# Optimization experiments

Hardware: AMD Instinct MI355X
Metric: run time of the kernel (lower is better)

Reference implementation:

```python
import jax, jax.numpy as jnp
import numpy as np

NHID = 256
NHEADS = 8
HEAD_F = NHID // NHEADS  # GAT per-head out_features
ALPHA = 0.1              # GAT LeakyReLU slope
NEG = -9e15


def _leaky(x, slope):
    return jnp.where(x >= 0, x, slope * x)


def _cnorm(x, axis):
    # matches Norm.compute_norm: (x - mean) / (std_unbiased + 1e-6)
    m = jnp.mean(x, axis=axis, keepdims=True)
    s = jnp.std(x, axis=axis, keepdims=True, ddof=1)
    return (x - m) / (s + 1e-6)


def _norm(x):
    # Norm('bn') forward: per-sample normalize over features (dim=1 of x[i]) then nodes (dim=0)
    return _cnorm(_cnorm(x, axis=2), axis=1)


def setup_inputs() -> dict:
    key = jax.random.key(0)
    ks = jax.random.split(key, 12)
    B, N, E, H, D = 4, 1024, NHID, NHEADS, HEAD_F

    def xavier(k, shape, gain=1.414):
        fan_in, fan_out = shape[-2], shape[-1]
        a = gain * np.sqrt(6.0 / (fan_in + fan_out))
        return jax.random.uniform(k, shape, jnp.float32, -a, a)

    return {
        "x": jax.random.normal(ks[0], (B, N, E), jnp.float32),
        "src": jax.random.normal(ks[1], (N, B, E), jnp.float32),
        "adj": jax.random.randint(ks[2], (B, N, N), 0, 2, jnp.int32),
        "Wg": xavier(ks[3], (H, E, D)),                 # per-head GAT W
        "a1": xavier(ks[4], (H, D, 1))[..., 0],         # a[:D]
        "a2": xavier(ks[5], (H, D, 1))[..., 0],         # a[D:]
        "lin_w": xavier(ks[6], (E, E), gain=1.0),
        "lin_b": jnp.zeros((E,), jnp.float32),
        "in_proj_w": xavier(ks[7], (3 * E, E), gain=1.0),
        "in_proj_b": jnp.zeros((3 * E,), jnp.float32),
        "out_proj_w": xavier(ks[8], (E, E), gain=1.0),
        "out_proj_b": jnp.zeros((E,), jnp.float32),
    }


def reference(x, src, adj, Wg, a1, a2, lin_w, lin_b, in_proj_w, in_proj_b, out_proj_w, out_proj_b):
    B, N, E = x.shape
    H, D = NHEADS, HEAD_F

    # --- multi-head dense GAT (all heads vectorized) ---
    Wh = jnp.einsum("bnf,hfd->hbnd", x, Wg)                      # [H,B,N,D]
    s1 = jnp.einsum("hbnd,hd->hbn", Wh, a1)                      # a1 . Wh_i
    s2 = jnp.einsum("hbnd,hd->hbn", Wh, a2)                      # a2 . Wh_j
    e = _leaky(s1[..., :, None] + s2[..., None, :], ALPHA)       # [H,B,N,N]
    e = jnp.where(adj[None] > 0, e, NEG)
    attn = jax.nn.softmax(e, axis=-1)                            # [H,B,N,N]
    hp = _leaky(jnp.einsum("hbnm,hbmd->hbnd", attn, Wh), 0.01)   # F.leaky_relu default

    x = x + jnp.transpose(hp, (1, 2, 0, 3)).reshape(B, N, H * D)
    e_out = jnp.mean(attn, axis=0)                               # [B,N,N]

    # --- norm1 -> linear -> norm2 ---
    x = _norm(x) @ lin_w.T + lin_b
    x = _norm(x)

    # --- nn.MultiheadAttention(query=x, key=x, value=src) ---
    srcb = jnp.transpose(src, (1, 0, 2))                         # [B,N,E]
    Wq, Wk, Wv = in_proj_w[:E], in_proj_w[E:2 * E], in_proj_w[2 * E:]
    bq, bk, bv = in_proj_b[:E], in_proj_b[E:2 * E], in_proj_b[2 * E:]
    Dh = E // H
    q = (x @ Wq.T + bq).reshape(B, N, H, Dh)
    k = (x @ Wk.T + bk).reshape(B, N, H, Dh)
    v = (srcb @ Wv.T + bv).reshape(B, N, H, Dh)
    scores = jnp.einsum("bqhd,bkhd->bhqk", q, k) / jnp.sqrt(jnp.float32(Dh))
    p = jax.nn.softmax(scores, axis=-1)
    o = jnp.einsum("bhqk,bkhd->bqhd", p, v).reshape(B, N, E)
    x = o @ out_proj_w.T + out_proj_b                            # [B,N,E]

    return (x, e_out)
```

## Files before the change

kernel.cpp:

```cpp
#include <hip/hip_runtime.h>
#include <hip/hip_bf16.h>

#define BIAS_OFF 196608
#define S1_OFF   198400
#define S2_OFF   231168
#define CS_OFF   263936
#define ST1_OFF  296704
#define ST2_OFF  298752
#define A_OFF    300800
#define MX_OFF   825088
#define RS_OFF   857856
#define PK_OFF   890624
#define B_OFF    1349376
#define C_OFF    2397952
#define FLAG_F   3446528

#define NEGC (-9.0e15f)

typedef __attribute__((ext_vector_type(8))) short bf16x8s;
typedef __attribute__((ext_vector_type(4))) float f32x4;

static __device__ __forceinline__ float bf2f(unsigned short u) {
  union { unsigned int i; float f; } v; v.i = ((unsigned int)u) << 16; return v.f;
}
static __device__ __forceinline__ unsigned short f2bf(float f) {
  union { float f; unsigned int u; } v; v.f = f;
  unsigned int r = (v.u + 0x7FFFu + ((v.u >> 16) & 1u)) >> 16;
  return (unsigned short)r;
}
static __device__ __forceinline__ float ldin(const void* p, long i, int bf) {
  return bf ? bf2f(((const unsigned short*)p)[i]) : ((const float*)p)[i];
}
static __device__ __forceinline__ unsigned short rdbf(const void* p, long i, int bf) {
  if (bf) return ((const unsigned short*)p)[i];
  return f2bf(((const float*)p)[i]);
}
static __device__ __forceinline__ void stout(void* p, long i, float v, int bf) {
  if (bf) ((unsigned short*)p)[i] = f2bf(v);
  else    ((float*)p)[i] = v;
}

__global__ __launch_bounds__(64) void detect_kernel(const unsigned short* x, int* flag) {
  int lane = threadIdx.x;
  unsigned short u = x[2 * lane];
  int e = (u >> 7) & 0xFF;
  bool good = (e >= 100 && e <= 140);
  unsigned long long m = __ballot(good);
  if (lane == 0) *flag = (__popcll(m) >= 48) ? 1 : 0;
}

__global__ __launch_bounds__(256) void packadj_kernel(const int* adj,
                                                      unsigned long long* pk) {
  int t = threadIdx.x, w = t >> 6, lane = t & 63;
  long row = blockIdx.x;
  #pragma unroll
  for (int j = 0; j < 4; ++j) {
    int m = t + 256*j;
    bool bit = adj[row*1024 + m] > 0;
    unsigned long long mask = __ballot(bit);
    if (lane == 0) pk[row*16 + w + 4*j] = mask;
  }
}

__global__ __launch_bounds__(256) void prep_kernel(
    const void* wg, const void* lin_w, const void* inp_w, const void* out_w,
    const void* lin_b, const void* inp_b, const void* out_b,
    const void* a1, const void* a2, float* ws, const int* flagp) {
  const int bf = *flagp;
  unsigned short* wbf = (unsigned short*)ws;
  int t = threadIdx.x;
  int f = blockIdx.x;
  int m = blockIdx.y;
  int dst = m*65536 + ((f >> 2)*256 + t)*4 + (f & 3);
  if (m == 0) {
    int h = t >> 5, d = t & 31;
    wbf[dst] = rdbf(wg, h*8192 + f*32 + d, bf);
  } else if (m == 1) wbf[dst] = rdbf(lin_w, t*256 + f, bf);
  else if (m == 2)   wbf[dst] = rdbf(inp_w, t*256 + f, bf);
  else if (m == 3)   wbf[dst] = rdbf(inp_w, (256 + t)*256 + f, bf);
  else if (m == 4)   wbf[dst] = rdbf(inp_w, (512 + t)*256 + f, bf);
  else if (m == 5)   wbf[dst] = rdbf(out_w, t*256 + f, bf);
  else if (f == 0) {
    ws[BIAS_OFF + t]        = ldin(lin_b, t, bf);
    ws[BIAS_OFF + 256 + t]  = ldin(inp_b, t, bf);
    ws[BIAS_OFF + 512 + t]  = ldin(inp_b, 256 + t, bf);
    ws[BIAS_OFF + 768 + t]  = ldin(inp_b, 512 + t, bf);
    ws[BIAS_OFF + 1024 + t] = ldin(out_b, t, bf);
    ws[BIAS_OFF + 1280 + t] = ldin(a1, t, bf);
    ws[BIAS_OFF + 1536 + t] = ldin(a2, t, bf);
  }
}

__global__ __launch_bounds__(256) void whs_kernel(const void* x, float* ws,
                                                  const int* flagp) {
  const int bf = *flagp;
  int t = threadIdx.x;
  int r0 = blockIdx.x * 8;
  __shared__ __align__(16) float U[8][256];
  #pragma unroll
  for (int r = 0; r < 8; ++r)
    U[r][t] = ldin(x, (long)(r0 + r)*256 + t, bf);
  __syncthreads();
  const ushort4* w4 = (const ushort4*)ws;
  float acc[8] = {0,0,0,0,0,0,0,0};
  for (int e4 = 0; e4 < 64; ++e4) {
    ushort4 u = w4[e4*256 + t];
    float w0 = bf2f(u.x), w1 = bf2f(u.y), w2 = bf2f(u.z), w3 = bf2f(u.w);
    #pragma unroll
    for (int r = 0; r < 8; ++r) {
      float4 uu = *(const float4*)&U[r][e4*4];
      acc[r] += uu.x*w0 + uu.y*w1 + uu.z*w2 + uu.w*w3;
    }
  }
  int h = t >> 5, d = t & 31;
  float a1v = ws[BIAS_OFF + 1280 + t];
  float a2v = ws[BIAS_OFF + 1536 + t];
  unsigned short wvals[8];
  #pragma unroll
  for (int r = 0; r < 8; ++r) {
    int row = r0 + r;
    wvals[r] = f2bf(acc[r]);
    float p1 = acc[r]*a1v, p2 = acc[r]*a2v;
    #pragma unroll
    for (int off = 16; off > 0; off >>= 1) {
      p1 += __shfl_xor(p1, off, 32);
      p2 += __shfl_xor(p2, off, 32);
    }
    if (d == 0) {
      ws[S1_OFF + h*4096 + row] = p1;
      ws[S2_OFF + h*4096 + row] = p2;
    }
  }
  {
    unsigned short* wht = (unsigned short*)(ws + A_OFF);
    int bb = r0 >> 10, nn = r0 & 1023;
    *(bf16x8s*)(wht + ((long)((h*4 + bb)*32 + d))*1024 + nn) = *(bf16x8s*)wvals;
  }
}

#define PB_S 1032
__global__ __launch_bounds__(512) void attn1a_kernel(const void* x, float* ws,
                                                     const int* flagp) {
  const int bf = *flagp;
  int t = threadIdx.x;
  int gid = blockIdx.x;
  int h = gid & 7;
  int b = (gid >> 3) & 3;
  int n0 = (gid >> 5) * 16;
  __shared__ __align__(16) float s2s[1024];
  __shared__ __align__(16) unsigned short Pb[16][PB_S];
  __shared__ __align__(16) float opart[8][16][17];
  int w = t >> 6, lane = t & 63;
  int m = lane & 15, quad = lane >> 4;
  const unsigned long long* pk = (const unsigned long long*)(ws + PK_OFF);
  const float* s2p = ws + S2_OFF + h*4096 + b*1024;
  #pragma unroll
  for (int j = 0; j < 2; ++j) s2s[t + 512*j] = s2p[t + 512*j];
  __syncthreads();
  #pragma unroll
  for (int rr = 0; rr < 2; ++rr) {
    int r = 2*w + rr;
    int rowi = __builtin_amdgcn_readfirstlane(b*1024 + n0 + r);
    const unsigned long long* prow = pk + (long)rowi * 16;
    float s1v = ws[S1_OFF + h*4096 + rowi];
    float p[16];
    float mx = -3.4e38f;
    #pragma unroll
    for (int j = 0; j < 16; ++j) {
      int mm = lane + 64*j;
      float ev = s1v + s2s[mm];
      ev = (ev >= 0.0f) ? ev : 0.1f*ev;
      ev = ((prow[j] >> lane) & 1ull) ? ev : NEGC;
      p[j] = ev;
      mx = fmaxf(mx, ev);
    }
    #pragma unroll
    for (int off = 32; off > 0; off >>= 1) mx = fmaxf(mx, __shfl_xor(mx, off));
    float s = 0.0f;
    #pragma unroll
    for (int j = 0; j < 16; ++j) { p[j] = __expf(p[j] - mx); s += p[j]; }
    #pragma unroll
    for (int off = 32; off > 0; off >>= 1) s += __shfl_xor(s, off);
    float rs = 1.0f / s;
    #pragma unroll
    for (int j = 0; j < 16; ++j)
      Pb[r][lane + 64*j] = f2bf(p[j] * rs);
    if (lane == 0) {
      ws[MX_OFF + h*4096 + rowi] = mx;
      ws[RS_OFF + h*4096 + rowi] = rs;
    }
  }
  __syncthreads();
  {
    const unsigned short* wht = (const unsigned short*)(ws + A_OFF);
    int ntile = w & 1;
    int ktbase = (w >> 1) * 8;
    int vd = ntile*16 + m;
    const unsigned short* wrow = wht + ((long)((h*4 + b)*32 + vd))*1024;
    f32x4 acc0 = {0.0f, 0.0f, 0.0f, 0.0f};
    f32x4 acc1 = {0.0f, 0.0f, 0.0f, 0.0f};
    #pragma unroll
    for (int kt2 = 0; kt2 < 4; ++kt2) {
      int kt = ktbase + 2*kt2;
      bf16x8s ap0 = *(const bf16x8s*)&Pb[m][kt*32 + quad*8];
      bf16x8s bw0 = *(const bf16x8s*)(wrow + kt*32 + quad*8);
      acc0 = __builtin_amdgcn_mfma_f32_16x16x32_bf16(ap0, bw0, acc0, 0, 0, 0);
      bf16x8s ap1 = *(const bf16x8s*)&Pb[m][(kt+1)*32 + quad*8];
      bf16x8s bw1 = *(const bf16x8s*)(wrow + (kt+1)*32 + quad*8);
      acc1 = __builtin_amdgcn_mfma_f32_16x16x32_bf16(ap1, bw1, acc1, 0, 0, 0);
    }
    f32x4 acc = acc0 + acc1;
    #pragma unroll
    for (int i = 0; i < 4; ++i)
      opart[w][quad*4 + i][m] = acc[i];
  }
  __syncthreads();
  {
    int r = t >> 5, dd = t & 31;
    int nt = dd >> 4, c = dd & 15;
    float sum = opart[nt][r][c] + opart[nt + 2][r][c]
              + opart[nt + 4][r][c] + opart[nt + 6][r][c];
    float hv = (sum >= 0.0f) ? sum : 0.01f*sum;
    long idx = (long)(b*1024 + n0 + r)*256 + h*32 + dd;
    ws[C_OFF + idx] = ldin(x, idx, bf) + hv;
  }
}

__global__ __launch_bounds__(256) void eout_kernel(float* ws, void* dout,
                                                   const int* flagp) {
  const int bf = *flagp;
  int t = threadIdx.x;
  int gid = blockIdx.x;
  int b = gid & 3;
  int n = gid >> 2;
  int row = b*1024 + n;
  int w = t >> 6, lane = t & 63;
  __shared__ float part[8];
  const unsigned long long* pk = (const unsigned long long*)(ws + PK_OFF);
  const unsigned long long* prow = pk + (long)row * 16;
  float v = ws[C_OFF + (long)row*256 + t];
  float s = v;
  #pragma unroll
  for (int off = 32; off > 0; off >>= 1) s += __shfl_xor(s, off);
  if (lane == 0) part[w] = s;
  __syncthreads();
  float mean = (part[0] + part[1] + part[2] + part[3]) * (1.0f/256.0f);
  float d = v - mean;
  float ss = d*d;
  #pragma unroll
  for (int off = 32; off > 0; off >>= 1) ss += __shfl_xor(ss, off);
  if (lane == 0) part[4 + w] = ss;
  __syncthreads();
  float inv = 1.0f / (sqrtf((part[4]+part[5]+part[6]+part[7]) * (1.0f/255.0f)) + 1e-6f);
  ws[B_OFF + (long)row*256 + t] = d * inv;
  float s1v[8], mxv[8], rsv[8];
  #pragma unroll
  for (int h = 0; h < 8; ++h) {
    s1v[h] = ws[S1_OFF + h*4096 + row];
    mxv[h] = ws[MX_OFF + h*4096 + row];
    rsv[h] = ws[RS_OFF + h*4096 + row];
  }
  const float* s2b = ws + S2_OFF + b*1024;
  #pragma unroll
  for (int j = 0; j < 4; ++j) {
    int m = t + 256*j;
    bool a = (prow[w + 4*j] >> lane) & 1ull;
    float acc = 0.0f;
    #pragma unroll
    for (int h = 0; h < 8; ++h) {
      float ev = s1v[h] + s2b[h*4096 + m];
      ev = (ev >= 0.0f) ? ev : 0.1f*ev;
      ev = a ? ev : NEGC;
      acc += rsv[h] * __expf(ev - mxv[h]);
    }
    stout(dout, 1048576L + (long)row*1024 + m, 0.125f*acc, bf);
  }
}

__global__ __launch_bounds__(256) void colstatsA_kernel(const float* in, float* cs) {
  int t = threadIdx.x;
  int j = blockIdx.x & 15;
  int b = blockIdx.x >> 4;
  float s = 0, ss = 0;
  for (int n = j*64; n < j*64 + 64; ++n) {
    float v = in[(b*1024 + n)*256 + t];
    s += v; ss += v*v;
  }
  cs[(b*16 + j)*256 + t] = s;
  cs[16384 + (b*16 + j)*256 + t] = ss;
}

__global__ __launch_bounds__(256) void colstatsB_kernel(const float* cs, float* st) {
  int t = threadIdx.x;
  int b = blockIdx.x;
  float s = 0, ss = 0;
  for (int j = 0; j < 16; ++j) {
    s  += cs[(b*16 + j)*256 + t];
    ss += cs[16384 + (b*16 + j)*256 + t];
  }
  float mean = s * (1.0f/1024.0f);
  float var = fmaxf((ss - s*mean) * (1.0f/1023.0f), 0.0f);
  st[b*256 + t] = mean;
  st[1024 + b*256 + t] = 1.0f / (sqrtf(var) + 1e-6f);
}

template<int IN_MODE, int RN, int OUTM, int ROWS>
__global__ __launch_bounds__(256) void gemm_kernel(const void* inp,
    const unsigned short* wmat, const float* bias, const float* st, void* outp,
    const int* flagp) {
  const int bf = *flagp;
  int t = threadIdx.x;
  int r0 = blockIdx.x * ROWS;
  __shared__ __align__(16) float U[ROWS][256];
  #pragma unroll
  for (int r = 0; r < ROWS; ++r) {
    int row = r0 + r;
    float v;
    if (IN_MODE == 0) {
      v = ((const float*)inp)[row*256 + t];
    } else if (IN_MODE == 1) {
      int b = row >> 10;
      v = (((const float*)inp)[row*256 + t] - st[b*256 + t]) * st[1024 + b*256 + t];
    } else if (IN_MODE == 2) {
      int b = row >> 10, n = row & 1023;
      v = ldin(inp, (long)(n*4 + b)*256 + t, bf);
    } else {
      int b = row >> 10, n = row & 1023;
      v = ((const float*)inp)[((b*8 + (t >> 5))*1024 + n)*32 + (t & 31)];
    }
    U[r][t] = v;
  }
  __syncthreads();
  float bv = bias[t];
  float acc[ROWS];
  #pragma unroll
  for (int r = 0; r < ROWS; ++r) acc[r] = bv;
  const ushort4* w4 = (const ushort4*)wmat;
  for (int e4 = 0; e4 < 64; ++e4) {
    ushort4 u = w4[e4*256 + t];
    float w0 = bf2f(u.x), w1 = bf2f(u.y), w2 = bf2f(u.z), w3 = bf2f(u.w);
    #pragma unroll
    for (int r = 0; r < ROWS; ++r) {
      float4 uu = *(const float4*)&U[r][e4*4];
      acc[r] += uu.x*w0 + uu.y*w1 + uu.z*w2 + uu.w*w3;
    }
  }
  if (RN == 0) {
    #pragma unroll
    for (int r = 0; r < ROWS; ++r) {
      int row = r0 + r;
      if (OUTM == 0) ((float*)outp)[row*256 + t] = acc[r];
      else if (OUTM == 1) stout(outp, (long)row*256 + t, acc[r], bf);
      else if (OUTM == 2) {
        int b = row >> 10, n = row & 1023;
        ((float*)outp)[((b*8 + (t >> 5))*1024 + n)*32 + (t & 31)] = acc[r];
      } else if (OUTM == 3) {
        int b = row >> 10, n = row & 1023;
        ((unsigned short*)outp)[((b*8 + (t >> 5))*1024 + n)*32 + (t & 31)] = f2bf(acc[r]);
      } else {
        int b = row >> 10, n = row & 1023;
        ((unsigned short*)outp)[((b*8 + (t >> 5))*32 + (t & 31))*1024 + n] = f2bf(acc[r]);
      }
    }
  } else {
    __syncthreads();
    #pragma unroll
    for (int r = 0; r < ROWS; ++r) U[r][t] = acc[r];
    __syncthreads();
    int w = t >> 6, lane = t & 63;
    for (int rr = w; rr < ROWS; rr += 4) {
      float vals[4]; float s = 0.0f;
      #pragma unroll
      for (int j = 0; j < 4; ++j) { vals[j] = U[rr][lane + 64*j]; s += vals[j]; }
      #pragma unroll
      for (int off = 32; off > 0; off >>= 1) s += __shfl_xor(s, off);
      float mean = s * (1.0f/256.0f);
      float ss = 0.0f;
      #pragma unroll
      for (int j = 0; j < 4; ++j) { float d = vals[j] - mean; ss += d*d; }
      #pragma unroll
      for (int off = 32; off > 0; off >>= 1) ss += __shfl_xor(ss, off);
      float inv = 1.0f / (sqrtf(ss * (1.0f/255.0f)) + 1e-6f);
      #pragma unroll
      for (int j = 0; j < 4; ++j)
        ((float*)outp)[(r0 + rr)*256 + lane + 64*j] = (vals[j] - mean) * inv;
    }
  }
}

#define SPS 1036
__global__ __launch_bounds__(512) void attn2_kernel(float* ws) {
  int t = threadIdx.x;
  int gid = blockIdx.x;
  int h = gid & 7;
  int b = (gid >> 3) & 3;
  int n0 = (gid >> 5) << 4;
  __shared__ __align__(16) float Sp[16*SPS];
  __shared__ __align__(16) float opart[8][16][17];
  float* qq = ws + A_OFF;
  const unsigned short* kk = (const unsigned short*)(ws + B_OFF);
  const unsigned short* vt = (const unsigned short*)(ws + C_OFF);
  int base_bh = (b*8 + h)*1024;
  int w = t >> 6, lane = t & 63;
  int m = lane & 15, quad = lane >> 4;
  const float scl = 0.17677669529663687f;
  {
    const float* qp = qq + (base_bh + n0 + m)*32 + quad*8;
    bf16x8s aq;
    #pragma unroll
    for (int j = 0; j < 8; ++j) ((unsigned short*)&aq)[j] = f2bf(qp[j]);
    f32x4 zero = {0.0f, 0.0f, 0.0f, 0.0f};
    #pragma unroll
    for (int kt = 0; kt < 8; ++kt) {
      int kbase = w*128 + kt*16;
      bf16x8s bk = *(const bf16x8s*)(kk + (base_bh + kbase + m)*32 + quad*8);
      f32x4 d = __builtin_amdgcn_mfma_f32_16x16x32_bf16(aq, bk, zero, 0, 0, 0);
      int key = kbase + m;
      #pragma unroll
      for (int i = 0; i < 4; ++i)
        Sp[(quad*4 + i)*SPS + key] = d[i] * scl;
    }
  }
  __syncthreads();
  #pragma unroll
  for (int rr = 0; rr < 2; ++rr) {
    int r = 2*w + rr;
    float* Sr = Sp + r*SPS;
    float p[16];
    #pragma unroll
    for (int j = 0; j < 16; ++j) p[j] = Sr[lane + 64*j];
    float mx = -3.4e38f;
    #pragma unroll
    for (int j = 0; j < 16; ++j) mx = fmaxf(mx, p[j]);
    #pragma unroll
    for (int off = 32; off > 0; off >>= 1) mx = fmaxf(mx, __shfl_xor(mx, off));
    float s = 0.0f;
    #pragma unroll
    for (int j = 0; j < 16; ++j) { p[j] = __expf(p[j] - mx); s += p[j]; }
    #pragma unroll
    for (int off = 32; off > 0; off >>= 1) s += __shfl_xor(s, off);
    float rs = 1.0f / s;
    unsigned short* Pr = (unsigned short*)Sr;
    #pragma unroll
    for (int j = 0; j < 16; ++j)
      Pr[lane + 64*j] = f2bf(p[j] * rs);
  }
  __syncthreads();
  {
    int ntile = w & 1;
    int ktbase = (w >> 1) * 8;
    int vd = ntile*16 + m;
    const unsigned short* vrow = vt + base_bh*32 + vd*1024;
    const unsigned short* P0 = (const unsigned short*)Sp + m*(SPS*2);
    f32x4 acc0 = {0.0f, 0.0f, 0.0f, 0.0f};
    f32x4 acc1 = {0.0f, 0.0f, 0.0f, 0.0f};
    #pragma unroll
    for (int kt2 = 0; kt2 < 4; ++kt2) {
      int kt = ktbase + 2*kt2;
      bf16x8s ap0 = *(const bf16x8s*)(P0 + kt*32 + quad*8);
      bf16x8s bv0 = *(const bf16x8s*)(vrow + kt*32 + quad*8);
      acc0 = __builtin_amdgcn_mfma_f32_16x16x32_bf16(ap0, bv0, acc0, 0, 0, 0);
      bf16x8s ap1 = *(const bf16x8s*)(P0 + (kt+1)*32 + quad*8);
      bf16x8s bv1 = *(const bf16x8s*)(vrow + (kt+1)*32 + quad*8);
      acc1 = __builtin_amdgcn_mfma_f32_16x16x32_bf16(ap1, bv1, acc1, 0, 0, 0);
    }
    f32x4 acc = acc0 + acc1;
    #pragma unroll
    for (int i = 0; i < 4; ++i)
      opart[w][quad*4 + i][m] = acc[i];
  }
  __syncthreads();
  {
    int r = t >> 5, d = t & 31;
    int nt = d >> 4, c = d & 15;
    float sum = opart[nt][r][c] + opart[nt + 2][r][c]
              + opart[nt + 4][r][c] + opart[nt + 6][r][c];
    qq[(base_bh + n0 + r)*32 + d] = sum;
  }
}

extern "C" void kernel_launch(void* const* d_in, const int* in_sizes, int n_in,
                              void* d_out, int out_size, void* d_ws, size_t ws_size,
                              hipStream_t stream) {
  const void* x   = d_in[0];
  const void* src = d_in[1];
  const int* adj  = (const int*)d_in[2];
  const void* wg  = d_in[3];
  const void* a1  = d_in[4];
  const void* a2  = d_in[5];
  const void* lw  = d_in[6];
  const void* lb  = d_in[7];
  const void* ipw = d_in[8];
  const void* ipb = d_in[9];
  const void* opw = d_in[10];
  const void* opb = d_in[11];
  float* ws = (float*)d_ws;
  const unsigned short* wbf = (const unsigned short*)d_ws;
  int* flagp = (int*)(ws + FLAG_F);

  detect_kernel<<<1, 64, 0, stream>>>((const unsigned short*)x, flagp);
  prep_kernel<<<dim3(256, 7), 256, 0, stream>>>(wg, lw, ipw, opw, lb, ipb, opb,
                                                a1, a2, ws, flagp);
  packadj_kernel<<<4096, 256, 0, stream>>>(adj,
      (unsigned long long*)(ws + PK_OFF));
  whs_kernel<<<512, 256, 0, stream>>>(x, ws, flagp);
  attn1a_kernel<<<2048, 512, 0, stream>>>(x, ws, flagp);
  eout_kernel<<<4096, 256, 0, stream>>>(ws, d_out, flagp);
  colstatsA_kernel<<<64, 256, 0, stream>>>(ws + B_OFF, ws + CS_OFF);
  colstatsB_kernel<<<4, 256, 0, stream>>>(ws + CS_OFF, ws + ST1_OFF);
  gemm_kernel<1,1,0,4><<<1024, 256, 0, stream>>>(ws + B_OFF, wbf + 1*65536,
      ws + BIAS_OFF, ws + ST1_OFF, ws + C_OFF, flagp);
  colstatsA_kernel<<<64, 256, 0, stream>>>(ws + C_OFF, ws + CS_OFF);
  colstatsB_kernel<<<4, 256, 0, stream>>>(ws + CS_OFF, ws + ST2_OFF);
  gemm_kernel<1,0,2,4><<<1024, 256, 0, stream>>>(ws + C_OFF, wbf + 2*65536,
      ws + BIAS_OFF + 256, ws + ST2_OFF, ws + A_OFF, flagp);
  gemm_kernel<1,0,3,4><<<1024, 256, 0, stream>>>(ws + C_OFF, wbf + 3*65536,
      ws + BIAS_OFF + 512, ws + ST2_OFF, ws + B_OFF, flagp);
  gemm_kernel<2,0,4,4><<<1024, 256, 0, stream>>>(src, wbf + 4*65536,
      ws + BIAS_OFF + 768, nullptr, ws + C_OFF, flagp);
  attn2_kernel<<<2048, 512, 0, stream>>>(ws);
  gemm_kernel<3,0,1,4><<<1024, 256, 0, stream>>>(ws + A_OFF, wbf + 5*65536,
      ws + BIAS_OFF + 1024, nullptr, d_out, flagp);
}
```

Measured before the change: 299.6 us.

## Replace scalar FMA GEMMs with split-bf16 MFMA GEMMs and fuse Q/K projections

Rewrites the dense projection GEMMs to use 16x16x32 bf16 MFMA instructions. Activations are split into high and low bf16 parts so the results stay close to fp32 accuracy. Q and K projections are fused into one kernel that shares the staged input tile, and the weight layout in prep changes to row-major per output column to match. Column-stat reduction is spread over more blocks with a larger partial buffer, now placed in the MX region. The cost is doubled MFMA work for the hi/lo split and fewer blocks per GEMM.

```diff
diff --git a/kernel.cpp b/kernel.cpp
--- a/kernel.cpp
+++ b/kernel.cpp
@@ -71,16 +71,18 @@
   int t = threadIdx.x;
   int f = blockIdx.x;
   int m = blockIdx.y;
-  int dst = m*65536 + ((f >> 2)*256 + t)*4 + (f & 3);
   if (m == 0) {
     int h = t >> 5, d = t & 31;
+    int dst = ((f >> 2)*256 + t)*4 + (f & 3);
     wbf[dst] = rdbf(wg, h*8192 + f*32 + d, bf);
-  } else if (m == 1) wbf[dst] = rdbf(lin_w, t*256 + f, bf);
-  else if (m == 2)   wbf[dst] = rdbf(inp_w, t*256 + f, bf);
-  else if (m == 3)   wbf[dst] = rdbf(inp_w, (256 + t)*256 + f, bf);
-  else if (m == 4)   wbf[dst] = rdbf(inp_w, (512 + t)*256 + f, bf);
-  else if (m == 5)   wbf[dst] = rdbf(out_w, t*256 + f, bf);
-  else if (f == 0) {
+  } else if (m <= 5) {
+    int dst = m*65536 + t*256 + f;
+    if (m == 1)      wbf[dst] = rdbf(lin_w, t*256 + f, bf);
+    else if (m == 2) wbf[dst] = rdbf(inp_w, t*256 + f, bf);
+    else if (m == 3) wbf[dst] = rdbf(inp_w, (256 + t)*256 + f, bf);
+    else if (m == 4) wbf[dst] = rdbf(inp_w, (512 + t)*256 + f, bf);
+    else             wbf[dst] = rdbf(out_w, t*256 + f, bf);
+  } else if (f == 0) {
     ws[BIAS_OFF + t]        = ldin(lin_b, t, bf);
     ws[BIAS_OFF + 256 + t]  = ldin(inp_b, t, bf);
     ws[BIAS_OFF + 512 + t]  = ldin(inp_b, 256 + t, bf);
@@ -279,24 +281,24 @@
 
 __global__ __launch_bounds__(256) void colstatsA_kernel(const float* in, float* cs) {
   int t = threadIdx.x;
-  int j = blockIdx.x & 15;
-  int b = blockIdx.x >> 4;
+  int j = blockIdx.x & 63;
+  int b = blockIdx.x >> 6;
   float s = 0, ss = 0;
-  for (int n = j*64; n < j*64 + 64; ++n) {
+  for (int n = j*16; n < j*16 + 16; ++n) {
     float v = in[(b*1024 + n)*256 + t];
     s += v; ss += v*v;
   }
-  cs[(b*16 + j)*256 + t] = s;
-  cs[16384 + (b*16 + j)*256 + t] = ss;
+  cs[(b*64 + j)*256 + t] = s;
+  cs[65536 + (b*64 + j)*256 + t] = ss;
 }
 
 __global__ __launch_bounds__(256) void colstatsB_kernel(const float* cs, float* st) {
   int t = threadIdx.x;
   int b = blockIdx.x;
   float s = 0, ss = 0;
-  for (int j = 0; j < 16; ++j) {
-    s  += cs[(b*16 + j)*256 + t];
-    ss += cs[16384 + (b*16 + j)*256 + t];
+  for (int j = 0; j < 64; ++j) {
+    s  += cs[(b*64 + j)*256 + t];
+    ss += cs[65536 + (b*64 + j)*256 + t];
   }
   float mean = s * (1.0f/1024.0f);
   float var = fmaxf((ss - s*mean) * (1.0f/1023.0f), 0.0f);
@@ -304,74 +306,138 @@
   st[1024 + b*256 + t] = 1.0f / (sqrtf(var) + 1e-6f);
 }
 
-template<int IN_MODE, int RN, int OUTM, int ROWS>
-__global__ __launch_bounds__(256) void gemm_kernel(const void* inp,
-    const unsigned short* wmat, const float* bias, const float* st, void* outp,
-    const int* flagp) {
+template<int IN_MODE, int RN, int OUTM, int CS>
+__global__ __launch_bounds__(512) void gemm2_kernel(const void* inp,
+    const unsigned short* wmat, const unsigned short* wmat2,
+    const float* bias, const float* bias2, const float* st,
+    void* outp, const int* flagp) {
   const int bf = *flagp;
   int t = threadIdx.x;
-  int r0 = blockIdx.x * ROWS;
-  __shared__ __align__(16) float U[ROWS][256];
-  #pragma unroll
-  for (int r = 0; r < ROWS; ++r) {
-    int row = r0 + r;
-    float v;
-    if (IN_MODE == 0) {
-      v = ((const float*)inp)[row*256 + t];
-    } else if (IN_MODE == 1) {
-      int b = row >> 10;
-      v = (((const float*)inp)[row*256 + t] - st[b*256 + t]) * st[1024 + b*256 + t];
+  int gid = blockIdx.x;
+  int rowg = (CS == 2) ? (gid >> 1) : gid;
+  int colbase = (CS == 2) ? ((gid & 1) * 128) : 0;
+  int r0 = rowg * 16;
+  __shared__ __align__(16) unsigned short Usm[2*16*264];
+  unsigned short (*Uh)[264] = (unsigned short (*)[264])Usm;
+  unsigned short (*Ul)[264] = (unsigned short (*)[264])(Usm + 16*264);
+  {
+    int srow = t >> 5;
+    int e0 = (t & 31) * 8;
+    long grow = r0 + srow;
+    float v[8];
+    if (IN_MODE == 1) {
+      int b = (int)(grow >> 10);
+      const float* ip = (const float*)inp + grow*256 + e0;
+      const float* mp = st + b*256 + e0;
+      const float* vp = st + 1024 + b*256 + e0;
+      #pragma unroll
+      for (int j = 0; j < 8; ++j) v[j] = (ip[j] - mp[j]) * vp[j];
     } else if (IN_MODE == 2) {
-      int b = row >> 10, n = row & 1023;
-      v = ldin(inp, (long)(n*4 + b)*256 + t, bf);
+      int b = (int)(grow >> 10), n = (int)(grow & 1023);
+      #pragma unroll
+      for (int j = 0; j < 8; ++j)
+        v[j] = ldin(inp, (long)(n*4 + b)*256 + e0 + j, bf);
     } else {
-      int b = row >> 10, n = row & 1023;
-      v = ((const float*)inp)[((b*8 + (t >> 5))*1024 + n)*32 + (t & 31)];
-    }
-    U[r][t] = v;
-  }
-  __syncthreads();
-  float bv = bias[t];
-  float acc[ROWS];
-  #pragma unroll
-  for (int r = 0; r < ROWS; ++r) acc[r] = bv;
-  const ushort4* w4 = (const ushort4*)wmat;
-  for (int e4 = 0; e4 < 64; ++e4) {
-    ushort4 u = w4[e4*256 + t];
-    float w0 = bf2f(u.x), w1 = bf2f(u.y), w2 = bf2f(u.z), w3 = bf2f(u.w);
-    #pragma unroll
-    for (int r = 0; r < ROWS; ++r) {
-      float4 uu = *(const float4*)&U[r][e4*4];
-      acc[r] += uu.x*w0 + uu.y*w1 + uu.z*w2 + uu.w*w3;
-    }
-  }
-  if (RN == 0) {
-    #pragma unroll
-    for (int r = 0; r < ROWS; ++r) {
-      int row = r0 + r;
-      if (OUTM == 0) ((float*)outp)[row*256 + t] = acc[r];
-      else if (OUTM == 1) stout(outp, (long)row*256 + t, acc[r], bf);
-      else if (OUTM == 2) {
-        int b = row >> 10, n = row & 1023;
-        ((float*)outp)[((b*8 + (t >> 5))*1024 + n)*32 + (t & 31)] = acc[r];
-      } else if (OUTM == 3) {
-        int b = row >> 10, n = row & 1023;
-        ((unsigned short*)outp)[((b*8 + (t >> 5))*1024 + n)*32 + (t & 31)] = f2bf(acc[r]);
-      } else {
-        int b = row >> 10, n = row & 1023;
-        ((unsigned short*)outp)[((b*8 + (t >> 5))*32 + (t & 31))*1024 + n] = f2bf(acc[r]);
+      int b = (int)(grow >> 10), n = (int)(grow & 1023);
+      const float* ip = (const float*)inp
+          + ((long)(b*8 + (e0 >> 5))*1024 + n)*32 + (e0 & 31);
+      #pragma unroll
+      for (int j = 0; j < 8; ++j) v[j] = ip[j];
+    }
+    unsigned short hv[8], lv[8];
+    #pragma unroll
+    for (int j = 0; j < 8; ++j) {
+      hv[j] = f2bf(v[j]);
+      lv[j] = f2bf(v[j] - bf2f(hv[j]));
+    }
+    *(bf16x8s*)&Uh[srow][e0] = *(bf16x8s*)hv;
+    *(bf16x8s*)&Ul[srow][e0] = *(bf16x8s*)lv;
+  }
+  __syncthreads();
+  int w = t >> 6, lane = t & 63, m = lane & 15, quad = lane >> 4;
+  const int NT = (CS == 1) ? 2 : 1;
+  f32x4 accs[2];
+  f32x4 acck;
+  #pragma unroll
+  for (int nt = 0; nt < NT; ++nt) {
+    int o = colbase + w*16 + nt*128 + m;
+    const unsigned short* wp = wmat + o*256 + quad*8;
+    f32x4 ah_acc = {0,0,0,0}, al_acc = {0,0,0,0};
+    f32x4 kh_acc = {0,0,0,0}, kl_acc = {0,0,0,0};
+    const unsigned short* wp2 = (OUTM == 5) ? (wmat2 + o*256 + quad*8) : wp;
+    #pragma unroll
+    for (int kt = 0; kt < 8; ++kt) {
+      bf16x8s ah = *(const bf16x8s*)&Uh[m][kt*32 + quad*8];
+      bf16x8s al = *(const bf16x8s*)&Ul[m][kt*32 + quad*8];
+      bf16x8s bw = *(const bf16x8s*)(wp + kt*32);
+      ah_acc = __builtin_amdgcn_mfma_f32_16x16x32_bf16(ah, bw, ah_acc, 0, 0, 0);
+      al_acc = __builtin_amdgcn_mfma_f32_16x16x32_bf16(al, bw, al_acc, 0, 0, 0);
+      if (OUTM == 5) {
+        bf16x8s bw2 = *(const bf16x8s*)(wp2 + kt*32);
+        kh_acc = __builtin_amdgcn_mfma_f32_16x16x32_bf16(ah, bw2, kh_acc, 0, 0, 0);
+        kl_acc = __builtin_amdgcn_mfma_f32_16x16x32_bf16(al, bw2, kl_acc, 0, 0, 0);
       }
     }
-  } else {
+    accs[nt] = ah_acc + al_acc;
+    if (OUTM == 5) acck = kh_acc + kl_acc;
+    if (RN == 0) {
+      float bv = bias[o];
+      if constexpr (OUTM == 0) {
+        #pragma unroll
+        for (int i = 0; i < 4; ++i) {
+          long row = r0 + quad*4 + i;
+          ((float*)outp)[row*256 + o] = accs[nt][i] + bv;
+        }
+      } else if constexpr (OUTM == 1) {
+        #pragma unroll
+        for (int i = 0; i < 4; ++i) {
+          long row = r0 + quad*4 + i;
+          stout(outp, row*256 + o, accs[nt][i] + bv, bf);
+        }
+      } else if constexpr (OUTM == 4) {
+        int h = o >> 5, d = o & 31;
+        #pragma unroll
+        for (int i = 0; i < 4; ++i) {
+          long row = r0 + quad*4 + i;
+          int b = (int)(row >> 10), n = (int)(row & 1023);
+          ((unsigned short*)outp)[((long)((b*8 + h)*32 + d))*1024 + n]
+              = f2bf(accs[nt][i] + bv);
+        }
+      } else if constexpr (OUTM == 5) {
+        float* wsf = (float*)outp;
+        float* qhm = wsf + A_OFF;
+        unsigned short* khm = (unsigned short*)(wsf + B_OFF);
+        float bq = bias[o], bk = bias2[o];
+        int h = o >> 5, d = o & 31;
+        #pragma unroll
+        for (int i = 0; i < 4; ++i) {
+          long row = r0 + quad*4 + i;
+          int b = (int)(row >> 10), n = (int)(row & 1023);
+          long idx = ((long)((b*8 + h)*1024 + n))*32 + d;
+          qhm[idx] = accs[nt][i] + bq;
+          khm[idx] = f2bf(acck[i] + bk);
+        }
+      }
+    }
+  }
+  if constexpr (RN == 1) {
     __syncthreads();
-    #pragma unroll
-    for (int r = 0; r < ROWS; ++r) U[r][t] = acc[r];
+    float (*O)[264] = (float (*)[264])Usm;
+    #pragma unroll
+    for (int nt = 0; nt < NT; ++nt) {
+      int oc = colbase + w*16 + nt*128 + m;
+      float bv = bias[oc];
+      #pragma unroll
+      for (int i = 0; i < 4; ++i)
+        O[quad*4 + i][oc] = accs[nt][i] + bv;
+    }
     __syncthreads();
-    int w = t >> 6, lane = t & 63;
-    for (int rr = w; rr < ROWS; rr += 4) {
+    #pragma unroll
+    for (int rr = 0; rr < 2; ++rr) {
+      int r = 2*w + rr;
       float vals[4]; float s = 0.0f;
       #pragma unroll
-      for (int j = 0; j < 4; ++j) { vals[j] = U[rr][lane + 64*j]; s += vals[j]; }
+      for (int j = 0; j < 4; ++j) { vals[j] = O[r][lane + 64*j]; s += vals[j]; }
       #pragma unroll
       for (int off = 32; off > 0; off >>= 1) s += __shfl_xor(s, off);
       float mean = s * (1.0f/256.0f);
@@ -383,7 +449,7 @@
       float inv = 1.0f / (sqrtf(ss * (1.0f/255.0f)) + 1e-6f);
       #pragma unroll
       for (int j = 0; j < 4; ++j)
-        ((float*)outp)[(r0 + rr)*256 + lane + 64*j] = (vals[j] - mean) * inv;
+        ((float*)outp)[(long)(r0 + r)*256 + lane + 64*j] = (vals[j] - mean) * inv;
     }
   }
 }
@@ -506,19 +572,18 @@
   whs_kernel<<<512, 256, 0, stream>>>(x, ws, flagp);
   attn1a_kernel<<<2048, 512, 0, stream>>>(x, ws, flagp);
   eout_kernel<<<4096, 256, 0, stream>>>(ws, d_out, flagp);
-  colstatsA_kernel<<<64, 256, 0, stream>>>(ws + B_OFF, ws + CS_OFF);
-  colstatsB_kernel<<<4, 256, 0, stream>>>(ws + CS_OFF, ws + ST1_OFF);
-  gemm_kernel<1,1,0,4><<<1024, 256, 0, stream>>>(ws + B_OFF, wbf + 1*65536,
-      ws + BIAS_OFF, ws + ST1_OFF, ws + C_OFF, flagp);
-  colstatsA_kernel<<<64, 256, 0, stream>>>(ws + C_OFF, ws + CS_OFF);
-  colstatsB_kernel<<<4, 256, 0, stream>>>(ws + CS_OFF, ws + ST2_OFF);
-  gemm_kernel<1,0,2,4><<<1024, 256, 0, stream>>>(ws + C_OFF, wbf + 2*65536,
-      ws + BIAS_OFF + 256, ws + ST2_OFF, ws + A_OFF, flagp);
-  gemm_kernel<1,0,3,4><<<1024, 256, 0, stream>>>(ws + C_OFF, wbf + 3*65536,
-      ws + BIAS_OFF + 512, ws + ST2_OFF, ws + B_OFF, flagp);
-  gemm_kernel<2,0,4,4><<<1024, 256, 0, stream>>>(src, wbf + 4*65536,
-      ws + BIAS_OFF + 768, nullptr, ws + C_OFF, flagp);
+  colstatsA_kernel<<<256, 256, 0, stream>>>(ws + B_OFF, ws + MX_OFF);
+  colstatsB_kernel<<<4, 256, 0, stream>>>(ws + MX_OFF, ws + ST1_OFF);
+  gemm2_kernel<1,1,0,1><<<256, 512, 0, stream>>>(ws + B_OFF, wbf + 1*65536,
+      nullptr, ws + BIAS_OFF, nullptr, ws + ST1_OFF, ws + C_OFF, flagp);
+  colstatsA_kernel<<<256, 256, 0, stream>>>(ws + C_OFF, ws + MX_OFF);
+  colstatsB_kernel<<<4, 256, 0, stream>>>(ws + MX_OFF, ws + ST2_OFF);
+  gemm2_kernel<1,0,5,2><<<512, 512, 0, stream>>>(ws + C_OFF, wbf + 2*65536,
+      wbf + 3*65536, ws + BIAS_OFF + 256, ws + BIAS_OFF + 512, ws + ST2_OFF,
+      ws, flagp);
+  gemm2_kernel<2,0,4,2><<<512, 512, 0, stream>>>(src, wbf + 4*65536,
+      nullptr, ws + BIAS_OFF + 768, nullptr, nullptr, ws + C_OFF, flagp);
   attn2_kernel<<<2048, 512, 0, stream>>>(ws);
-  gemm_kernel<3,0,1,4><<<1024, 256, 0, stream>>>(ws + A_OFF, wbf + 5*65536,
-      ws + BIAS_OFF + 1024, nullptr, d_out, flagp);
-}
+  gemm2_kernel<3,0,1,2><<<512, 512, 0, stream>>>(ws + A_OFF, wbf + 5*65536,
+      nullptr, ws + BIAS_OFF + 1024, nullptr, nullptr, d_out, flagp);
+}
```

New measurement: 255.2 us. -14.8%, faster.
